# Kernel tuning notes

Measured on AMD Instinct MI355X. Metric: run time of the kernel, lower is better.

Reference implementation:

```python
import jax, jax.numpy as jnp
import numpy as np
from jax import lax

D = 1024
H = 1024


def setup_inputs() -> dict:
    key = jax.random.key(0)
    ks = jax.random.split(key, 6)
    N, T = 256, 64
    x = jax.random.normal(ks[0], (N, T, D), dtype=jnp.float32)
    A = jax.random.normal(ks[1], (N, H, 4, 4), dtype=jnp.float32)
    Wx = jax.random.normal(ks[2], (D, 4 * H), dtype=jnp.float32) / np.sqrt(D)
    Wh = jax.random.normal(ks[3], (H, 4 * H), dtype=jnp.float32) / np.sqrt(H)
    Wattn = jax.random.normal(ks[4], (H, 4 * H), dtype=jnp.float32) / np.sqrt(H)
    b = jnp.zeros((4 * H,), dtype=jnp.float32)
    return {"x": x, "A": A, "Wx": Wx, "Wh": Wh, "Wattn": Wattn, "b": b}


def reference(x, A, Wx, Wh, Wattn, b):
    N, T, Din = x.shape
    Hh = A.shape[1]
    A_flat = A.reshape(N, Hh, -1)  # (N, H, 16)
    inv_sqrt_h = jnp.asarray(1.0 / np.sqrt(Hh), dtype=x.dtype)
    h0 = jnp.mean(A, axis=(2, 3))  # (N, H)
    c0 = h0

    def step(carry, xt):
        prev_h, prev_c = carry
        # dot-product attention over the 16 spatial positions
        scores = jnp.einsum('nh,nhp->np', prev_h, A_flat) * inv_sqrt_h
        w = jax.nn.softmax(scores, axis=-1)          # (N, 16)
        attn = jnp.einsum('nhp,np->nh', A_flat, w)   # (N, H)
        # fused LSTM gate preactivation
        a = xt @ Wx + prev_h @ Wh + attn @ Wattn + b  # (N, 4H)
        i, f, o, g = jnp.split(a, 4, axis=-1)
        next_c = jax.nn.sigmoid(f) * prev_c + jax.nn.sigmoid(i) * jnp.tanh(g)
        next_h = jax.nn.sigmoid(o) * jnp.tanh(next_c)
        return (next_h, next_c), next_h

    _, hs = lax.scan(step, (h0, c0), jnp.swapaxes(x, 0, 1))  # hs: (T, N, H)
    return jnp.swapaxes(hs, 0, 1)  # (N, T, H)
```

## Files before the change

### kernel.cpp

```cpp
#include <hip/hip_runtime.h>

typedef __bf16 bf16;
typedef bf16 bf16x8 __attribute__((ext_vector_type(8)));
typedef bf16 bf16x4 __attribute__((ext_vector_type(4)));
typedef float f32x4 __attribute__((ext_vector_type(4)));

#define NB 256
#define TS 64
#define DD 1024
#define HH 1024
#define NOUT 4096


static __device__ __forceinline__ void gload_lds16(const void* g, void* l) {
  __builtin_amdgcn_global_load_lds(
      (const __attribute__((address_space(1))) void*)g,
      (__attribute__((address_space(3))) void*)l, 16, 0, 0);
}

#define SWZ_ADD(v, imm) \
  (v) += __int_as_float(__builtin_amdgcn_ds_swizzle(__float_as_int(v), imm))
#define SWZ_MAX(v, imm) \
  (v) = fmaxf(v, __int_as_float(__builtin_amdgcn_ds_swizzle(__float_as_int(v), imm)))

__global__ __launch_bounds__(256) void convert_bf(const float* __restrict__ in,
                                                  bf16* __restrict__ o) {
  const size_t gid = (size_t)blockIdx.x * 256 + threadIdx.x;
  bf16x8 v;
#pragma unroll
  for (int j = 0; j < 8; ++j) v[j] = (bf16)in[gid * 8 + j];
  *(bf16x8*)(o + gid * 8) = v;
}

__global__ __launch_bounds__(256) void convert_wt2(const float* __restrict__ W,
                                                   bf16* __restrict__ Wt) {
  __shared__ bf16 lb[8 * 4096];
  const int kb = blockIdx.x;
  const int kt = kb >> 2, group = kb & 3;
  const int tid = threadIdx.x;
#pragma unroll
  for (int qq = 0; qq < 32; ++qq) {
    const int chunk = qq * 256 + tid;
    const int row = chunk >> 10;
    const int colb = (chunk & 1023) * 4;
    const f32x4 v = *(const f32x4*)(W + (size_t)(kb * 8 + row) * NOUT + colb);
#pragma unroll
    for (int e = 0; e < 4; ++e) {
      const int co = colb + e;
      const int hh = co & 1023, g = co >> 10;
      const int cx = (hh >> 4) * 64 + (hh & 15) * 4 + g;
      lb[row * 4096 + cx] = (bf16)v[e];
    }
  }
  __syncthreads();
  const int tau = tid;
  bf16* wbase = Wt + (size_t)(tau * 32 + kt) * 512 + group * 16 * 8;
#pragma unroll
  for (int c = 0; c < 16; ++c) {
    const int cx = tau * 16 + c;
    bf16x8 o;
#pragma unroll
    for (int j = 0; j < 8; ++j) o[j] = lb[j * 4096 + cx];
    *(bf16x8*)(wbase + c * 8) = o;
  }
}

__global__ __launch_bounds__(1024) void transpose_A(const float* __restrict__ A,
                                                    bf16* __restrict__ At) {
  __shared__ float lt[1024 * 17];
  const int n = blockIdx.x, u = threadIdx.x;
  const float* ar = A + ((size_t)n * HH + u) * 16;
#pragma unroll
  for (int q = 0; q < 4; ++q) {
    f32x4 v = *(const f32x4*)(ar + q * 4);
#pragma unroll
    for (int r = 0; r < 4; ++r) lt[u * 17 + q * 4 + r] = v[r];
  }
  __syncthreads();
  const int p = u >> 6, seg = u & 63;
  bf16x8 o0, o1;
#pragma unroll
  for (int j = 0; j < 8; ++j) {
    o0[j] = (bf16)lt[(seg * 16 + j) * 17 + p];
    o1[j] = (bf16)lt[(seg * 16 + 8 + j) * 17 + p];
  }
  bf16* dst = At + (size_t)(n * 16 + p) * 1024 + seg * 16;
  *(bf16x8*)dst = o0;
  *(bf16x8*)(dst + 8) = o1;
}

template <int MODE>
__global__ __launch_bounds__(256, 3) void gemm128(const bf16* __restrict__ Am,
                                                  const bf16* __restrict__ Bt,
                                                  bf16* __restrict__ C,
                                                  const float* __restrict__ bias) {
  __shared__ __align__(16) bf16 astg[2][8 * 512];
  __shared__ __align__(16) bf16 bstg[2][8 * 512];
  const int b = blockIdx.x;
  const int ct = (b & 7) * 4 + ((b >> 3) & 3);
  const int rt = b >> 5;
  const int tid = threadIdx.x, lane = tid & 63, wid = tid >> 6;
  const int wr = wid >> 1, wc = wid & 1;

  const bf16* gA[2];
  const bf16* gB[2];
  int lA[2], lB[2];
#pragma unroll
  for (int e = 0; e < 2; ++e) {
    const int mt = wid * 2 + e;
    gA[e] = Am + (size_t)(rt * 128 + mt * 16 + (lane & 15)) * 1024 + (lane >> 4) * 8;
    lA[e] = mt * 512;
    gB[e] = Bt + ((size_t)(ct * 8 + mt) * 32) * 512 + lane * 8;
    lB[e] = mt * 512;
  }
  f32x4 acc[4][4];
#pragma unroll
  for (int i = 0; i < 4; ++i)
#pragma unroll
    for (int j = 0; j < 4; ++j) acc[i][j] = (f32x4){0, 0, 0, 0};

#pragma unroll
  for (int e = 0; e < 2; ++e) {
    gload_lds16(gA[e], &astg[0][lA[e]]);
    gload_lds16(gB[e], &bstg[0][lB[e]]);
  }
  for (int it = 0; it < 32; ++it) {
    __syncthreads();
    if (it < 31) {
#pragma unroll
      for (int e = 0; e < 2; ++e) {
        gload_lds16(gA[e] + (it + 1) * 32, &astg[(it + 1) & 1][lA[e]]);
        gload_lds16(gB[e] + (size_t)(it + 1) * 512, &bstg[(it + 1) & 1][lB[e]]);
      }
    }
    const bf16* ab = astg[it & 1];
    const bf16* bb = bstg[it & 1];
    bf16x8 af[4], bfr[4];
#pragma unroll
    for (int i = 0; i < 4; ++i) af[i] = *(const bf16x8*)(ab + (wr * 4 + i) * 512 + lane * 8);
#pragma unroll
    for (int j = 0; j < 4; ++j) bfr[j] = *(const bf16x8*)(bb + (wc * 4 + j) * 512 + lane * 8);
#pragma unroll
    for (int i = 0; i < 4; ++i)
#pragma unroll
      for (int j = 0; j < 4; ++j)
        acc[i][j] = __builtin_amdgcn_mfma_f32_16x16x32_bf16(af[i], bfr[j], acc[i][j], 0, 0, 0);
  }
#pragma unroll
  for (int j = 0; j < 4; ++j) {
    const int col = ct * 128 + wc * 64 + j * 16 + (lane & 15);
    float bv = 0.f;
    if (MODE == 0) {
      const int rem = col & 63;
      bv = bias[(rem & 3) * HH + (col >> 6) * 16 + (rem >> 2)];
    }
#pragma unroll
    for (int i = 0; i < 4; ++i) {
      const int row0 = rt * 128 + wr * 64 + i * 16 + (lane >> 4) * 4;
#pragma unroll
      for (int r = 0; r < 4; ++r) {
        const int row = row0 + r;
        size_t idx;
        if (MODE == 0) idx = ((size_t)(row & 63) * NB + (row >> 6)) * NOUT + col;
        else           idx = (size_t)(row >> 4) * (NOUT * 16) + (size_t)col * 16 + (row & 15);
        C[idx] = (bf16)(acc[i][j][r] + bv);
      }
    }
  }
}

__global__ __launch_bounds__(1024) void init_kernel(const float* __restrict__ A,
                                                    float* __restrict__ c_ws,
                                                    bf16* __restrict__ Aop0,
                                                    float* __restrict__ s0) {
  __shared__ float h_sh[1024];
  __shared__ float scA[16], scB[16];
  const int n = (blockIdx.x & 7) * 32 + (blockIdx.x >> 3);
  const int u = threadIdx.x;
  const float* arow = A + ((size_t)n * HH + u) * 16;
  float h0 = 0.f;
#pragma unroll
  for (int p = 0; p < 16; ++p) h0 += arow[p];
  h0 *= 0.0625f;
  c_ws[(n << 10) + u] = h0;
  h_sh[u] = h0;
  Aop0[(n << 10) + u] = (bf16)h0;
  __syncthreads();
  const int lane = u & 63, w = u >> 6;
  const float* ap = A + (size_t)n * (HH * 16) + w;
  float s = 0.f;
#pragma unroll
  for (int i = 0; i < 16; ++i) {
    const int idx = lane + 64 * i;
    s = fmaf(h_sh[idx], ap[(size_t)idx * 16], s);
  }
  SWZ_ADD(s, 0x041F); SWZ_ADD(s, 0x081F); SWZ_ADD(s, 0x101F);
  SWZ_ADD(s, 0x201F); SWZ_ADD(s, 0x401F);
  if (lane == 0) scA[w] = s;
  else if (lane == 32) scB[w] = s;
  __syncthreads();
  if (u < 16) s0[n * 16 + u] = scA[u] + scB[u];
}

#define STEP_SMEM 65536
__global__ __launch_bounds__(512, 4) void step_kernel(
    const bf16* __restrict__ Aop_cur, bf16* __restrict__ Aop_nxt,
    const bf16* __restrict__ Wh_t, const bf16* __restrict__ xWx2,
    const bf16* __restrict__ G2, const float* __restrict__ s_cur,
    float* __restrict__ s_nxt, float* __restrict__ s_zro,
    const bf16* __restrict__ A_bf, float* __restrict__ c_ws,
    float* __restrict__ out, const int t) {
  __shared__ __align__(16) char smem[STEP_SMEM];
  __shared__ float w_sh[512];
  bf16* astg = (bf16*)smem;
  float* red = (float*)smem;

  const int b = blockIdx.x;
  const int xcd = b & 7;
  const int ht = xcd * 8 + ((b >> 3) & 7);
  const int rt = b >> 6;
  const int tid = threadIdx.x, lane = tid & 63, wid = tid >> 6;
  const int kg = wid >> 1, ow = wid & 1;
  const int nloc = tid >> 4, hl = tid & 15;
  const int n = rt * 32 + nloc, h = ht * 16 + hl;

  float ss = s_cur[n * 16 + hl];

#pragma unroll
  for (int e = 0; e < 8; ++e) {
    const int tau = wid * 8 + e;
    const int tkg = tau >> 4, tmt = (tau >> 3) & 1, tks = tau & 7;
    const bf16* src = Aop_cur +
        (size_t)(rt * 32 + tmt * 16 + (lane & 15)) * 1024 +
        tkg * 256 + tks * 32 + (lane >> 4) * 8;
    gload_lds16(src, astg + tkg * 8192 + (tmt * 8 + tks) * 512);
  }

  bf16x8 gq[8];
  {
    const bf16* Gp = G2 + (size_t)n * (NOUT * 16) + (size_t)(ht * 64 + hl * 4) * 16;
#pragma unroll
    for (int e = 0; e < 8; ++e) gq[e] = *(const bf16x8*)(Gp + e * 8);
  }
  const bf16x4 xv = *(const bf16x4*)(xWx2 + (size_t)t * (NB * NOUT) +
                                     (size_t)n * NOUT + ht * 64 + hl * 4);
  if (tid < 8) s_zro[b * 8 + tid] = 0.f;

  {
    ss *= 0.03125f;
    float m = ss;
    SWZ_MAX(m, 0x041F); SWZ_MAX(m, 0x081F); SWZ_MAX(m, 0x101F); SWZ_MAX(m, 0x201F);
    const float e = expf(ss - m);
    float su = e;
    SWZ_ADD(su, 0x041F); SWZ_ADD(su, 0x081F); SWZ_ADD(su, 0x101F); SWZ_ADD(su, 0x201F);
    w_sh[tid] = e / su;
  }
  __syncthreads();

  const bf16* gB0 = Wh_t + ((size_t)(ht * 4 + ow * 2 + 0) * 32 + kg * 8) * 512 + lane * 8;
  const bf16* gB1 = Wh_t + ((size_t)(ht * 4 + ow * 2 + 1) * 32 + kg * 8) * 512 + lane * 8;
  f32x4 a00 = {0, 0, 0, 0}, a01 = {0, 0, 0, 0}, a10 = {0, 0, 0, 0}, a11 = {0, 0, 0, 0};
  {
    const bf16* ab = astg + kg * 8192;
    bf16x8 bc0 = *(const bf16x8*)gB0;
    bf16x8 bc1 = *(const bf16x8*)gB1;
    __builtin_amdgcn_s_setprio(1);
#pragma unroll
    for (int ks = 0; ks < 8; ++ks) {
      bf16x8 bn0, bn1;
      if (ks < 7) {
        bn0 = *(const bf16x8*)(gB0 + (ks + 1) * 512);
        bn1 = *(const bf16x8*)(gB1 + (ks + 1) * 512);
      }
      const bf16x8 f0 = *(const bf16x8*)(ab + ks * 512 + lane * 8);
      const bf16x8 f1 = *(const bf16x8*)(ab + (8 + ks) * 512 + lane * 8);
      a00 = __builtin_amdgcn_mfma_f32_16x16x32_bf16(f0, bc0, a00, 0, 0, 0);
      a01 = __builtin_amdgcn_mfma_f32_16x16x32_bf16(f0, bc1, a01, 0, 0, 0);
      a10 = __builtin_amdgcn_mfma_f32_16x16x32_bf16(f1, bc0, a10, 0, 0, 0);
      a11 = __builtin_amdgcn_mfma_f32_16x16x32_bf16(f1, bc1, a11, 0, 0, 0);
      if (ks < 7) { bc0 = bn0; bc1 = bn1; }
    }
    __builtin_amdgcn_s_setprio(0);
  }
  __syncthreads();

  {
    const int cb = kg * 64 + ow * 32 + (lane & 15);
    const int nb = (lane >> 4) * 4;
    *(f32x4*)&red[(cb)*36 + nb] = a00;
    *(f32x4*)&red[(cb + 16) * 36 + nb] = a01;
    *(f32x4*)&red[(cb)*36 + nb + 16] = a10;
    *(f32x4*)&red[(cb + 16) * 36 + nb + 16] = a11;
  }
  __syncthreads();

  f32x4 gv = {0, 0, 0, 0};
#pragma unroll
  for (int k2 = 0; k2 < 4; ++k2)
#pragma unroll
    for (int g = 0; g < 4; ++g) gv[g] += red[(k2 * 64 + hl * 4 + g) * 36 + nloc];
#pragma unroll
  for (int g = 0; g < 4; ++g) {
    float a0 = 0.f;
#pragma unroll
    for (int p = 0; p < 8; ++p) a0 = fmaf(w_sh[nloc * 16 + p], (float)gq[g * 2][p], a0);
#pragma unroll
    for (int p = 0; p < 8; ++p) a0 = fmaf(w_sh[nloc * 16 + 8 + p], (float)gq[g * 2 + 1][p], a0);
    gv[g] += a0;
  }
  const float ai = gv[0] + (float)xv[0];
  const float af = gv[1] + (float)xv[1];
  const float ao = gv[2] + (float)xv[2];
  const float ag = gv[3] + (float)xv[3];
  const float cold = c_ws[(n << 10) + h];
  const float si = 1.f / (1.f + expf(-ai));
  const float sf = 1.f / (1.f + expf(-af));
  const float so = 1.f / (1.f + expf(-ao));
  const float cn = sf * cold + si * tanhf(ag);
  const float hn = so * tanhf(cn);
  c_ws[(n << 10) + h] = cn;
  out[((size_t)n * TS + t) * HH + h] = hn;
  Aop_nxt[(n << 10) + h] = (bf16)hn;

  if (t < TS - 1) {
    __syncthreads();
    const bf16* arow = A_bf + ((size_t)n * HH + h) * 16;
    const bf16x8 av0 = *(const bf16x8*)arow;
    const bf16x8 av1 = *(const bf16x8*)(arow + 8);
#pragma unroll
    for (int r = 0; r < 8; ++r) {
      red[(nloc * 16 + r) * 17 + hl] = hn * (float)av0[r];
      red[(nloc * 16 + 8 + r) * 17 + hl] = hn * (float)av1[r];
    }
    __syncthreads();
    const float* r2 = &red[(nloc * 16 + hl) * 17];
    float s = 0.f;
#pragma unroll
    for (int q = 0; q < 16; ++q) s += r2[q];
    atomicAdd(&s_nxt[n * 16 + hl], s);
  }
}

extern "C" void kernel_launch(void* const* d_in, const int* in_sizes, int n_in,
                              void* d_out, int out_size, void* d_ws, size_t ws_size,
                              hipStream_t stream) {
  const float* x     = (const float*)d_in[0];
  const float* A     = (const float*)d_in[1];
  const float* Wx    = (const float*)d_in[2];
  const float* Wh    = (const float*)d_in[3];
  const float* Wattn = (const float*)d_in[4];
  const float* bias  = (const float*)d_in[5];
  float* out = (float*)d_out;
  char* ws = (char*)d_ws;
  bf16* Wh_t   = (bf16*)(ws + 0);
  bf16* Wat_t  = (bf16*)(ws + 8388608);
  bf16* At     = (bf16*)(ws + 16777216);
  bf16* A_bf   = (bf16*)(ws + 25165824);
  bf16* xWx2   = (bf16*)(ws + 33554432);
  bf16* G2     = (bf16*)(ws + 167772160);
  bf16* x_bf   = (bf16*)(ws + 201326592);
  bf16* Wxt    = (bf16*)(ws + 234881024);
  bf16* Aop0   = (bf16*)(ws + 243269632);
  bf16* Aop1   = (bf16*)(ws + 243793920);
  float* s0    = (float*)(ws + 244318208);
  float* s1    = (float*)(ws + 244334592);
  float* s2    = (float*)(ws + 244350976);
  float* c_ws  = (float*)(ws + 244367360);

  hipMemsetAsync(s1, 0, 16384, stream);
  convert_bf<<<8192, 256, 0, stream>>>(x, x_bf);
  convert_bf<<<2048, 256, 0, stream>>>(A, A_bf);
  convert_wt2<<<128, 256, 0, stream>>>(Wx, Wxt);
  convert_wt2<<<128, 256, 0, stream>>>(Wh, Wh_t);
  convert_wt2<<<128, 256, 0, stream>>>(Wattn, Wat_t);
  gemm128<0><<<4096, 256, 0, stream>>>(x_bf, Wxt, xWx2, bias);
  transpose_A<<<256, 1024, 0, stream>>>(A, At);
  gemm128<1><<<1024, 256, 0, stream>>>(At, Wat_t, G2, nullptr);
  init_kernel<<<256, 1024, 0, stream>>>(A, c_ws, Aop0, s0);
  for (int t = 0; t < TS; ++t) {
    float* scur = (t % 3 == 0) ? s0 : (t % 3 == 1) ? s1 : s2;
    float* snxt = (t % 3 == 0) ? s1 : (t % 3 == 1) ? s2 : s0;
    float* szro = (t % 3 == 0) ? s2 : (t % 3 == 1) ? s0 : s1;
    step_kernel<<<512, 512, 0, stream>>>((t & 1) ? Aop1 : Aop0,
                                         (t & 1) ? Aop0 : Aop1, Wh_t, xWx2,
                                         G2, scur, snxt, szro, A_bf, c_ws,
                                         out, t);
  }
}
```

Before: 1.415 ms.

## Fuse A preprocessing kernels and transpose x during bf16 conversion

Result: no change. 1.399 ms (-1.1%).

```diff
diff --git a/kernel.cpp b/kernel.cpp
--- a/kernel.cpp
+++ b/kernel.cpp
@@ -23,13 +23,85 @@
 #define SWZ_MAX(v, imm) \
   (v) = fmaxf(v, __int_as_float(__builtin_amdgcn_ds_swizzle(__float_as_int(v), imm)))
 
-__global__ __launch_bounds__(256) void convert_bf(const float* __restrict__ in,
-                                                  bf16* __restrict__ o) {
-  const size_t gid = (size_t)blockIdx.x * 256 + threadIdx.x;
+__global__ __launch_bounds__(256) void convert_x(const float* __restrict__ x,
+                                                 bf16* __restrict__ xb) {
+  const int gid = blockIdx.x * 256 + threadIdx.x;
+  const int t = gid >> 15;
+  const int rem = gid & 32767;
+  const int n = rem >> 7;
+  const int d = (rem & 127) * 8;
+  const float* src = x + ((size_t)n * TS + t) * DD + d;
   bf16x8 v;
 #pragma unroll
-  for (int j = 0; j < 8; ++j) v[j] = (bf16)in[gid * 8 + j];
-  *(bf16x8*)(o + gid * 8) = v;
+  for (int j = 0; j < 8; ++j) v[j] = (bf16)src[j];
+  *(bf16x8*)(xb + (size_t)gid * 8) = v;
+}
+
+__global__ __launch_bounds__(1024) void prep_A(const float* __restrict__ A,
+                                               bf16* __restrict__ A_bf,
+                                               bf16* __restrict__ At,
+                                               float* __restrict__ c_ws,
+                                               bf16* __restrict__ Aop0,
+                                               float* __restrict__ s0) {
+  __shared__ float lt[1024 * 17];
+  __shared__ float h_sh[1024];
+  __shared__ float scA[16], scB[16];
+  const int n = (blockIdx.x & 7) * 32 + (blockIdx.x >> 3);
+  const int u = threadIdx.x;
+  const float* ar = A + ((size_t)n * HH + u) * 16;
+  float a[16];
+#pragma unroll
+  for (int q = 0; q < 4; ++q) {
+    const f32x4 v = *(const f32x4*)(ar + q * 4);
+#pragma unroll
+    for (int r = 0; r < 4; ++r) {
+      a[q * 4 + r] = v[r];
+      lt[u * 17 + q * 4 + r] = v[r];
+    }
+  }
+  {
+    bf16x8 b0, b1;
+#pragma unroll
+    for (int j = 0; j < 8; ++j) { b0[j] = (bf16)a[j]; b1[j] = (bf16)a[8 + j]; }
+    bf16* abf = A_bf + ((size_t)n * HH + u) * 16;
+    *(bf16x8*)abf = b0;
+    *(bf16x8*)(abf + 8) = b1;
+  }
+  float h0 = 0.f;
+#pragma unroll
+  for (int p = 0; p < 16; ++p) h0 += a[p];
+  h0 *= 0.0625f;
+  c_ws[(n << 10) + u] = h0;
+  h_sh[u] = h0;
+  Aop0[(n << 10) + u] = (bf16)h0;
+  __syncthreads();
+  {
+    const int p = u >> 6, seg = u & 63;
+    bf16x8 o0, o1;
+#pragma unroll
+    for (int j = 0; j < 8; ++j) {
+      o0[j] = (bf16)lt[(seg * 16 + j) * 17 + p];
+      o1[j] = (bf16)lt[(seg * 16 + 8 + j) * 17 + p];
+    }
+    bf16* dst = At + (size_t)(n * 16 + p) * 1024 + seg * 16;
+    *(bf16x8*)dst = o0;
+    *(bf16x8*)(dst + 8) = o1;
+  }
+  {
+    const int lane = u & 63, w = u >> 6;
+    float s = 0.f;
+#pragma unroll
+    for (int i = 0; i < 16; ++i) {
+      const int idx = lane + 64 * i;
+      s = fmaf(h_sh[idx], lt[idx * 17 + w], s);
+    }
+    SWZ_ADD(s, 0x041F); SWZ_ADD(s, 0x081F); SWZ_ADD(s, 0x101F);
+    SWZ_ADD(s, 0x201F); SWZ_ADD(s, 0x401F);
+    if (lane == 0) scA[w] = s;
+    else if (lane == 32) scB[w] = s;
+  }
+  __syncthreads();
+  if (u < 16) s0[n * 16 + u] = scA[u] + scB[u];
 }
 
 __global__ __launch_bounds__(256) void convert_wt2(const float* __restrict__ W,
@@ -65,32 +137,8 @@
   }
 }
 
-__global__ __launch_bounds__(1024) void transpose_A(const float* __restrict__ A,
-                                                    bf16* __restrict__ At) {
-  __shared__ float lt[1024 * 17];
-  const int n = blockIdx.x, u = threadIdx.x;
-  const float* ar = A + ((size_t)n * HH + u) * 16;
-#pragma unroll
-  for (int q = 0; q < 4; ++q) {
-    f32x4 v = *(const f32x4*)(ar + q * 4);
-#pragma unroll
-    for (int r = 0; r < 4; ++r) lt[u * 17 + q * 4 + r] = v[r];
-  }
-  __syncthreads();
-  const int p = u >> 6, seg = u & 63;
-  bf16x8 o0, o1;
-#pragma unroll
-  for (int j = 0; j < 8; ++j) {
-    o0[j] = (bf16)lt[(seg * 16 + j) * 17 + p];
-    o1[j] = (bf16)lt[(seg * 16 + 8 + j) * 17 + p];
-  }
-  bf16* dst = At + (size_t)(n * 16 + p) * 1024 + seg * 16;
-  *(bf16x8*)dst = o0;
-  *(bf16x8*)(dst + 8) = o1;
-}
-
 template <int MODE>
-__global__ __launch_bounds__(256, 3) void gemm128(const bf16* __restrict__ Am,
+__global__ __launch_bounds__(256, 4) void gemm128(const bf16* __restrict__ Am,
                                                   const bf16* __restrict__ Bt,
                                                   bf16* __restrict__ C,
                                                   const float* __restrict__ bias) {
@@ -161,45 +209,12 @@
       for (int r = 0; r < 4; ++r) {
         const int row = row0 + r;
         size_t idx;
-        if (MODE == 0) idx = ((size_t)(row & 63) * NB + (row >> 6)) * NOUT + col;
+        if (MODE == 0) idx = (size_t)row * NOUT + col;
         else           idx = (size_t)(row >> 4) * (NOUT * 16) + (size_t)col * 16 + (row & 15);
         C[idx] = (bf16)(acc[i][j][r] + bv);
       }
     }
   }
-}
-
-__global__ __launch_bounds__(1024) void init_kernel(const float* __restrict__ A,
-                                                    float* __restrict__ c_ws,
-                                                    bf16* __restrict__ Aop0,
-                                                    float* __restrict__ s0) {
-  __shared__ float h_sh[1024];
-  __shared__ float scA[16], scB[16];
-  const int n = (blockIdx.x & 7) * 32 + (blockIdx.x >> 3);
-  const int u = threadIdx.x;
-  const float* arow = A + ((size_t)n * HH + u) * 16;
-  float h0 = 0.f;
-#pragma unroll
-  for (int p = 0; p < 16; ++p) h0 += arow[p];
-  h0 *= 0.0625f;
-  c_ws[(n << 10) + u] = h0;
-  h_sh[u] = h0;
-  Aop0[(n << 10) + u] = (bf16)h0;
-  __syncthreads();
-  const int lane = u & 63, w = u >> 6;
-  const float* ap = A + (size_t)n * (HH * 16) + w;
-  float s = 0.f;
-#pragma unroll
-  for (int i = 0; i < 16; ++i) {
-    const int idx = lane + 64 * i;
-    s = fmaf(h_sh[idx], ap[(size_t)idx * 16], s);
-  }
-  SWZ_ADD(s, 0x041F); SWZ_ADD(s, 0x081F); SWZ_ADD(s, 0x101F);
-  SWZ_ADD(s, 0x201F); SWZ_ADD(s, 0x401F);
-  if (lane == 0) scA[w] = s;
-  else if (lane == 32) scB[w] = s;
-  __syncthreads();
-  if (u < 16) s0[n * 16 + u] = scA[u] + scB[u];
 }
 
 #define STEP_SMEM 65536
@@ -368,15 +383,13 @@
   float* c_ws  = (float*)(ws + 244367360);
 
   hipMemsetAsync(s1, 0, 16384, stream);
-  convert_bf<<<8192, 256, 0, stream>>>(x, x_bf);
-  convert_bf<<<2048, 256, 0, stream>>>(A, A_bf);
+  convert_x<<<8192, 256, 0, stream>>>(x, x_bf);
+  prep_A<<<256, 1024, 0, stream>>>(A, A_bf, At, c_ws, Aop0, s0);
   convert_wt2<<<128, 256, 0, stream>>>(Wx, Wxt);
   convert_wt2<<<128, 256, 0, stream>>>(Wh, Wh_t);
   convert_wt2<<<128, 256, 0, stream>>>(Wattn, Wat_t);
   gemm128<0><<<4096, 256, 0, stream>>>(x_bf, Wxt, xWx2, bias);
-  transpose_A<<<256, 1024, 0, stream>>>(A, At);
   gemm128<1><<<1024, 256, 0, stream>>>(At, Wat_t, G2, nullptr);
-  init_kernel<<<256, 1024, 0, stream>>>(A, c_ws, Aop0, s0);
   for (int t = 0; t < TS; ++t) {
     float* scur = (t % 3 == 0) ? s0 : (t % 3 == 1) ? s1 : s2;
     float* snxt = (t % 3 == 0) ? s1 : (t % 3 == 1) ? s2 : s0;
```
